# Performance work log

Measured on AMD Instinct MI355X. Metric: run time of the kernel, lower is better.

Reference implementation:

```python
import jax, jax.numpy as jnp
import numpy as np

LN_EPS = 1e-5      # torch.nn.LayerNorm default
NORM_EPS = 1e-12   # torch F.normalize default


def _layernorm(x, gamma, beta):
    mu = jnp.mean(x, axis=-1, keepdims=True)
    var = jnp.mean(jnp.square(x - mu), axis=-1, keepdims=True)
    return (x - mu) * jax.lax.rsqrt(var + LN_EPS) * gamma + beta


def _l2norm(x):
    # normalize over last (embedding) axis, matching F.normalize(dim=1) on [B,E,1,N]
    n = jnp.sqrt(jnp.sum(jnp.square(x), axis=-1, keepdims=True))
    return x / jnp.maximum(n, NORM_EPS)


def setup_inputs() -> dict:
    key = jax.random.key(0)
    ks = jax.random.split(key, 4)
    B, N, C, E = 8, 4096, 768, 768
    x = jax.random.normal(ks[0], (B, N, C), dtype=jnp.float32)
    w_qkv = jax.random.normal(ks[1], (C, 3 * E), dtype=jnp.float32) * (1.0 / np.sqrt(C))
    w_proj = jax.random.normal(ks[2], (E, C), dtype=jnp.float32) * (1.0 / np.sqrt(E))
    ln_in_g = jnp.ones((C,), jnp.float32)
    ln_in_b = jnp.zeros((C,), jnp.float32)
    ln_out_g = jnp.ones((E,), jnp.float32)
    ln_out_b = jnp.zeros((E,), jnp.float32)
    return {"x": x, "w_qkv": w_qkv, "w_proj": w_proj,
            "ln_in_g": ln_in_g, "ln_in_b": ln_in_b,
            "ln_out_g": ln_out_g, "ln_out_b": ln_out_b}


def reference(x, w_qkv, w_proj, ln_in_g, ln_in_b, ln_out_g, ln_out_b):
    # x: [B, N, C]
    h = _layernorm(x, ln_in_g, ln_in_b)
    qkv = h @ w_qkv                                  # [B, N, 3E]
    q, k, v = jnp.split(qkv, 3, axis=-1)             # each [B, N, E]
    phi_q = _l2norm(q)                               # per-token L2 over E
    phi_k = _l2norm(k)
    kv = jnp.sum(phi_k * v, axis=1)                  # [B, E] (sum over tokens N)
    attn = phi_q * kv[:, None, :]                    # [B, N, E]
    out = _layernorm(attn, ln_out_g, ln_out_b) @ w_proj  # [B, N, C]
    return out
```

## Files before the change

### kernel.cpp

```cpp
#include <hip/hip_runtime.h>
#include <hip/hip_bf16.h>
#include <cstdint>

typedef __bf16 bf16;
typedef __bf16 bf16x4 __attribute__((ext_vector_type(4)));
typedef __bf16 bf16x8 __attribute__((ext_vector_type(8)));
typedef float f32x4 __attribute__((ext_vector_type(4)));

#define GK 768
#define LN_EPS 1e-5f
#define NORM_EPS 1e-12f

__device__ __forceinline__ void gl_lds16(const void* g, void* l) {
  __builtin_amdgcn_global_load_lds(
      (__attribute__((address_space(1))) uint32_t*)(uintptr_t)g,
      (__attribute__((address_space(3))) uint32_t*)(uintptr_t)l,
      16, 0, 0);
}

__device__ __forceinline__ void blockReduce2w3(float& s, float& ss, float* sm) {
  #pragma unroll
  for (int o = 32; o > 0; o >>= 1) {
    s  += __shfl_down(s, o, 64);
    ss += __shfl_down(ss, o, 64);
  }
  int wave = threadIdx.x >> 6, lane = threadIdx.x & 63;
  if (lane == 0) { sm[wave] = s; sm[3 + wave] = ss; }
  __syncthreads();
  s  = sm[0] + sm[1] + sm[2];
  ss = sm[3] + sm[4] + sm[5];
  __syncthreads();
}

__global__ __launch_bounds__(256) void transpose_cvt(const float* __restrict__ w,
                                                     bf16* __restrict__ wt,
                                                     int R, int Ncols) {
  __shared__ float tile[32][33];
  int tx = threadIdx.x & 31, ty = threadIdx.x >> 5;
  int c0 = blockIdx.x * 32, r0 = blockIdx.y * 32;
  #pragma unroll
  for (int i = 0; i < 32; i += 8)
    tile[ty + i][tx] = w[(size_t)(r0 + ty + i) * Ncols + (c0 + tx)];
  __syncthreads();
  #pragma unroll
  for (int i = 0; i < 32; i += 8)
    wt[(size_t)(c0 + ty + i) * R + (r0 + tx)] = (bf16)tile[tx][ty + i];
}

__global__ __launch_bounds__(192) void ln_in_kernel(const float* __restrict__ x,
                                                    const float* __restrict__ g,
                                                    const float* __restrict__ b,
                                                    bf16* __restrict__ h) {
  __shared__ float sm[6];
  int row = blockIdx.x, t = threadIdx.x;
  const float* xr = x + (size_t)row * 768;
  float4 v = ((const float4*)xr)[t];
  float s  = v.x + v.y + v.z + v.w;
  float ss = v.x * v.x + v.y * v.y + v.z * v.z + v.w * v.w;
  blockReduce2w3(s, ss, sm);
  float mu  = s * (1.0f / 768.0f);
  float inv = rsqrtf(ss * (1.0f / 768.0f) - mu * mu + LN_EPS);
  float4 gg = ((const float4*)g)[t];
  float4 bb = ((const float4*)b)[t];
  bf16x4 o;
  o[0] = (bf16)((v.x - mu) * inv * gg.x + bb.x);
  o[1] = (bf16)((v.y - mu) * inv * gg.y + bb.y);
  o[2] = (bf16)((v.z - mu) * inv * gg.z + bb.z);
  o[3] = (bf16)((v.w - mu) * inv * gg.w + bb.w);
  ((bf16x4*)(h + (size_t)row * 768))[t] = o;
}


#define SWZ(x) ((x) ^ ((((x) >> 7) & 7) << 4))

#define SB0 __builtin_amdgcn_sched_barrier(0)
#define BARS do { SB0; __builtin_amdgcn_s_barrier(); SB0; } while (0)
#define LGKM(n) do { asm volatile("s_waitcnt lgkmcnt(" #n ")" ::: "memory"); SB0; } while (0)
#define VMC4 do { SB0; asm volatile("s_waitcnt vmcnt(4)" ::: "memory"); } while (0)
#define PRIO1 __builtin_amdgcn_s_setprio(1)
#define PRIO0 __builtin_amdgcn_s_setprio(0)

#define LDA1(base, mh, i, ks) \
  af[i][ks] = *(const bf16x8*)((base) + SWZ((wm * 128 + ((mh) * 4 + (i)) * 16 + llo) * 128 + (ks) * 64 + lhi * 16))

#define LDB1(base, n, ks) \
  bf[n][ks] = *(const bf16x8*)((base) + SWZ(((((n) >> 1) * 128 + wn * 32 + ((n) & 1) * 16 + llo) * 128 + (ks) * 64 + lhi * 16)))

#define MF1(mh, nh, i, jn, ks) \
  acc[(mh) * 4 + (i)][(nh) * 2 + (jn)] = __builtin_amdgcn_mfma_f32_16x16x32_bf16( \
      af[i][ks], bf[(nh) * 2 + (jn)][ks], acc[(mh) * 4 + (i)][(nh) * 2 + (jn)], 0, 0, 0)
#define MF8(mh, nh, ks) do { \
  MF1(mh, nh, 0, 0, ks); MF1(mh, nh, 0, 1, ks); MF1(mh, nh, 1, 0, ks); MF1(mh, nh, 1, 1, ks); \
  MF1(mh, nh, 2, 0, ks); MF1(mh, nh, 2, 1, ks); MF1(mh, nh, 3, 0, ks); MF1(mh, nh, 3, 1, ks); } while (0)

#define STA(b, q, kt) gl_lds16(A + srcA[q] + (kt) * 64, &As_[b][(q) * 4096 + wave * 512])
#define STB(b, q, kt) gl_lds16(Bt + srcB[q] + (kt) * 64, &Bs_[b][(q) * 4096 + wave * 512])

template <bool OUT_BF16>
__global__ __launch_bounds__(512, 2) void gemm8p(const bf16* __restrict__ A,
                                                 const bf16* __restrict__ Bt,
                                                 void* __restrict__ Cv,
                                                 int Nn, int NBN) {
  __shared__ __align__(16) bf16 As_[2][16384];
  __shared__ __align__(16) bf16 Bs_[2][16384];
  const int tid = threadIdx.x;
  const int wave = tid >> 6, lane = tid & 63;
  const int llo = lane & 15, lhi = lane >> 4;
  const int wm = wave >> 2, wn = wave & 3;

  const int nwg = gridDim.x, bid = blockIdx.x;
  const int wg = (bid & 7) * (nwg >> 3) + (bid >> 3);
  const int rb = wg / NBN, cb = wg - rb * NBN;
  const int brow = rb * 256, bcol = cb * 256;

  uint32_t srcA[4], srcB[4];
  #pragma unroll
  for (int q = 0; q < 4; ++q) {
    int d = q * 8192 + tid * 16;
    int a = SWZ(d);
    int r = a >> 7, c = (a & 127) >> 1;
    srcA[q] = (uint32_t)(brow + r) * GK + c;
    int nh = r >> 7, wnn = (r >> 5) & 3, r32 = r & 31;
    srcB[q] = (uint32_t)(bcol + wnn * 64 + nh * 32 + r32) * GK + c;
  }

  f32x4 acc[8][4];
  #pragma unroll
  for (int m = 0; m < 8; ++m)
    #pragma unroll
    for (int n = 0; n < 4; ++n) acc[m][n] = (f32x4){0.f, 0.f, 0.f, 0.f};

  bf16x8 af[4][2], bf[4][2];
  const char* As0 = (const char*)&As_[0][0];
  const char* As1 = (const char*)&As_[1][0];
  const char* Bs0 = (const char*)&Bs_[0][0];
  const char* Bs1 = (const char*)&Bs_[1][0];

  STA(0, 0, 0); STA(0, 1, 0); STA(0, 2, 0); STA(0, 3, 0);
  STB(0, 0, 0); STB(0, 1, 0); STB(0, 2, 0); STB(0, 3, 0);
  STA(1, 0, 1); STA(1, 2, 1); STB(1, 0, 1); STB(1, 1, 1);
  SB0;
  asm volatile("s_waitcnt vmcnt(4)" ::: "memory");
  __builtin_amdgcn_s_barrier();
  SB0;

  for (int j = 0; j < 6; ++j) {
    const int t1 = 2 * j + 1, t2 = 2 * j + 2, t3 = 2 * j + 3;
    LDA1(As0, 0, 0, 0); LDA1(As0, 0, 1, 0); LDA1(As0, 0, 2, 0); LDA1(As0, 0, 3, 0);
    LDB1(Bs0, 0, 0);    LDB1(Bs0, 1, 0);
    SB0;
    LDA1(As0, 0, 0, 1); LDA1(As0, 0, 1, 1); LDA1(As0, 0, 2, 1); LDA1(As0, 0, 3, 1);
    LDB1(Bs0, 0, 1);    LDB1(Bs0, 1, 1);
    SB0;
    LDB1(Bs0, 2, 0); LDB1(Bs0, 3, 0); LDB1(Bs0, 2, 1); LDB1(Bs0, 3, 1);
    STA(1, 1, t1); STA(1, 3, t1);
    BARS;
    LGKM(10); PRIO1; MF8(0, 0, 0);
    LGKM(4);  MF8(0, 0, 1); PRIO0;
    BARS;
    STB(1, 2, t1); STB(1, 3, t1);
    BARS;
    LGKM(0); PRIO1; MF8(0, 1, 0); MF8(0, 1, 1); PRIO0;
    BARS;
    LDA1(As0, 1, 0, 0); LDA1(As0, 1, 1, 0); LDA1(As0, 1, 2, 0); LDA1(As0, 1, 3, 0);
    SB0;
    LDA1(As0, 1, 0, 1); LDA1(As0, 1, 1, 1); LDA1(As0, 1, 2, 1); LDA1(As0, 1, 3, 1);
    STA(0, 0, t2); STA(0, 2, t2);
    BARS;
    LGKM(4); PRIO1; MF8(1, 0, 0);
    LGKM(0); MF8(1, 0, 1); PRIO0;
    BARS;
    STB(0, 0, t2); STB(0, 1, t2);
    BARS;
    PRIO1; MF8(1, 1, 0); MF8(1, 1, 1); PRIO0;
    VMC4;
    BARS;
    LDA1(As1, 0, 0, 0); LDA1(As1, 0, 1, 0); LDA1(As1, 0, 2, 0); LDA1(As1, 0, 3, 0);
    LDB1(Bs1, 0, 0);    LDB1(Bs1, 1, 0);
    SB0;
    LDA1(As1, 0, 0, 1); LDA1(As1, 0, 1, 1); LDA1(As1, 0, 2, 1); LDA1(As1, 0, 3, 1);
    LDB1(Bs1, 0, 1);    LDB1(Bs1, 1, 1);
    SB0;
    LDB1(Bs1, 2, 0); LDB1(Bs1, 3, 0); LDB1(Bs1, 2, 1); LDB1(Bs1, 3, 1);
    STA(0, 1, t2); STA(0, 3, t2);
    BARS;
    LGKM(10); PRIO1; MF8(0, 0, 0);
    LGKM(4);  MF8(0, 0, 1); PRIO0;
    BARS;
    STB(0, 2, t2); STB(0, 3, t2);
    BARS;
    LGKM(0); PRIO1; MF8(0, 1, 0); MF8(0, 1, 1); PRIO0;
    BARS;
    LDA1(As1, 1, 0, 0); LDA1(As1, 1, 1, 0); LDA1(As1, 1, 2, 0); LDA1(As1, 1, 3, 0);
    SB0;
    LDA1(As1, 1, 0, 1); LDA1(As1, 1, 1, 1); LDA1(As1, 1, 2, 1); LDA1(As1, 1, 3, 1);
    STA(1, 0, t3); STA(1, 2, t3);
    BARS;
    LGKM(4); PRIO1; MF8(1, 0, 0);
    LGKM(0); MF8(1, 0, 1); PRIO0;
    BARS;
    STB(1, 0, t3); STB(1, 1, t3);
    BARS;
    PRIO1; MF8(1, 1, 0); MF8(1, 1, 1); PRIO0;
    VMC4;
    BARS;
  }

  #pragma unroll
  for (int m = 0; m < 8; ++m) {
    #pragma unroll
    for (int n = 0; n < 4; ++n) {
      int row = brow + wm * 128 + m * 16 + lhi * 4;
      int col = bcol + wn * 64 + n * 16 + llo;
      #pragma unroll
      for (int r2 = 0; r2 < 4; ++r2) {
        if (OUT_BF16)
          ((bf16*)Cv)[(size_t)(row + r2) * Nn + col] = (bf16)acc[m][n][r2];
        else
          ((float*)Cv)[(size_t)(row + r2) * Nn + col] = acc[m][n][r2];
      }
    }
  }
}

__global__ __launch_bounds__(256) void kv_partial(const bf16* __restrict__ qkv,
                                                  float* __restrict__ kvp) {
  __shared__ float sm[4][768];
  int b = blockIdx.x >> 5, chunk = blockIdx.x & 31;
  int wave = threadIdx.x >> 6, lane = threadIdx.x & 63;
  const bf16* base = qkv + ((size_t)(b * 4096 + chunk * 128 + wave * 32)) * 2304;
  float acc[3][4] = {};
  for (int i = 0; i < 32; ++i) {
    const bf16* kr = base + (size_t)i * 2304 + 768;
    const bf16* vr = kr + 768;
    bf16x4 k4[3], v4[3];
    #pragma unroll
    for (int c = 0; c < 3; ++c) {
      k4[c] = *(const bf16x4*)(kr + c * 256 + lane * 4);
      v4[c] = *(const bf16x4*)(vr + c * 256 + lane * 4);
    }
    float ssk = 0.f;
    #pragma unroll
    for (int c = 0; c < 3; ++c)
      #pragma unroll
      for (int j = 0; j < 4; ++j) { float kf = (float)k4[c][j]; ssk += kf * kf; }
    #pragma unroll
    for (int off = 32; off > 0; off >>= 1) ssk += __shfl_xor(ssk, off, 64);
    float wi = 1.0f / fmaxf(sqrtf(ssk), NORM_EPS);
    #pragma unroll
    for (int c = 0; c < 3; ++c)
      #pragma unroll
      for (int j = 0; j < 4; ++j)
        acc[c][j] += (float)k4[c][j] * (float)v4[c][j] * wi;
  }
  #pragma unroll
  for (int c = 0; c < 3; ++c)
    #pragma unroll
    for (int j = 0; j < 4; ++j)
      sm[wave][c * 256 + lane * 4 + j] = acc[c][j];
  __syncthreads();
  int t = threadIdx.x;
  #pragma unroll
  for (int c = 0; c < 3; ++c) {
    int e = c * 256 + t;
    kvp[(size_t)blockIdx.x * 768 + e] = sm[0][e] + sm[1][e] + sm[2][e] + sm[3][e];
  }
}

__global__ __launch_bounds__(256) void kv_reduce(const float* __restrict__ kvp,
                                                 float* __restrict__ kv) {
  int i = blockIdx.x * 256 + threadIdx.x;
  int b = i / 768, e = i - b * 768;
  float s = 0.f;
  #pragma unroll
  for (int c = 0; c < 32; ++c) s += kvp[(size_t)(b * 32 + c) * 768 + e];
  kv[i] = s;
}

__global__ __launch_bounds__(192) void attn_ln_kernel(const bf16* __restrict__ qkv,
                                                      const float* __restrict__ kv,
                                                      const float* __restrict__ g,
                                                      const float* __restrict__ b,
                                                      bf16* __restrict__ a) {
  __shared__ float sm[6];
  int row = blockIdx.x, t = threadIdx.x;
  int bt = row >> 12;
  const bf16* qr = qkv + (size_t)row * 2304;
  bf16x4 q4 = ((const bf16x4*)qr)[t];
  float q0 = (float)q4[0], q1 = (float)q4[1], q2 = (float)q4[2], q3 = (float)q4[3];
  float sq = q0 * q0 + q1 * q1 + q2 * q2 + q3 * q3, dummy = 0.f;
  blockReduce2w3(sq, dummy, sm);
  float iq = 1.0f / fmaxf(sqrtf(sq), NORM_EPS);
  float4 kv4 = ((const float4*)(kv + bt * 768))[t];
  float4 av;
  av.x = q0 * iq * kv4.x;
  av.y = q1 * iq * kv4.y;
  av.z = q2 * iq * kv4.z;
  av.w = q3 * iq * kv4.w;
  float s  = av.x + av.y + av.z + av.w;
  float ss = av.x * av.x + av.y * av.y + av.z * av.z + av.w * av.w;
  blockReduce2w3(s, ss, sm);
  float mu  = s * (1.0f / 768.0f);
  float inv = rsqrtf(ss * (1.0f / 768.0f) - mu * mu + LN_EPS);
  float4 gg = ((const float4*)g)[t];
  float4 bb = ((const float4*)b)[t];
  bf16x4 o;
  o[0] = (bf16)((av.x - mu) * inv * gg.x + bb.x);
  o[1] = (bf16)((av.y - mu) * inv * gg.y + bb.y);
  o[2] = (bf16)((av.z - mu) * inv * gg.z + bb.z);
  o[3] = (bf16)((av.w - mu) * inv * gg.w + bb.w);
  ((bf16x4*)(a + (size_t)row * 768))[t] = o;
}

extern "C" void kernel_launch(void* const* d_in, const int* in_sizes, int n_in,
                              void* d_out, int out_size, void* d_ws, size_t ws_size,
                              hipStream_t stream) {
  const float* x      = (const float*)d_in[0];
  const float* w_qkv  = (const float*)d_in[1];
  const float* w_proj = (const float*)d_in[2];
  const float* g_in   = (const float*)d_in[3];
  const float* b_in   = (const float*)d_in[4];
  const float* g_out  = (const float*)d_in[5];
  const float* b_out  = (const float*)d_in[6];

  char* ws = (char*)d_ws;
  bf16*  wqkvt  = (bf16*)(ws);
  bf16*  wprojt = (bf16*)(ws + 3538944);
  bf16*  h      = (bf16*)(ws + 4718592);
  bf16*  qkv    = (bf16*)(ws + 55050240);
  float* kvp    = (float*)(ws + 206045184);
  float* kv     = (float*)(ws + 206831616);

  transpose_cvt<<<dim3(2304 / 32, 768 / 32), 256, 0, stream>>>(w_qkv, wqkvt, 768, 2304);
  transpose_cvt<<<dim3(768 / 32, 768 / 32), 256, 0, stream>>>(w_proj, wprojt, 768, 768);
  ln_in_kernel<<<32768, 192, 0, stream>>>(x, g_in, b_in, h);
  gemm8p<true><<<128 * 9, 512, 0, stream>>>(h, wqkvt, (void*)qkv, 2304, 9);
  kv_partial<<<256, 256, 0, stream>>>(qkv, kvp);
  kv_reduce<<<24, 256, 0, stream>>>(kvp, kv);
  attn_ln_kernel<<<32768, 192, 0, stream>>>(qkv, kv, g_out, b_out, h);
  gemm8p<false><<<128 * 3, 512, 0, stream>>>(h, wprojt, d_out, 768, 3);
}
```

Measured before the change: 292.6 us.

## Switch GEMMs to 32x32x16 MFMA and use 128-row tiles for projection

Replaces the 16x16x32 bf16 MFMA tiling in the pipelined GEMM with 32x32x16 MFMAs, changing the LDS fragment loads and the epilogue store mapping to fit. The GEMM is templated on M-tile count, and the output projection now uses 128-row tiles with a simpler double-buffered schedule, doubling its grid to 768 workgroups. The larger MFMA shape is meant to cut LDS fragment traffic per FLOP, and the smaller projection tiles are meant to fill more CUs. The trade-offs are a strided epilogue store pattern and less reuse per tile in the projection GEMM.

```diff
diff --git a/kernel.cpp b/kernel.cpp
--- a/kernel.cpp
+++ b/kernel.cpp
@@ -6,6 +6,7 @@
 typedef __bf16 bf16x4 __attribute__((ext_vector_type(4)));
 typedef __bf16 bf16x8 __attribute__((ext_vector_type(8)));
 typedef float f32x4 __attribute__((ext_vector_type(4)));
+typedef float f32x16 __attribute__((ext_vector_type(16)));
 
 #define GK 768
 #define LN_EPS 1e-5f
@@ -76,148 +77,190 @@
 #define SB0 __builtin_amdgcn_sched_barrier(0)
 #define BARS do { SB0; __builtin_amdgcn_s_barrier(); SB0; } while (0)
 #define LGKM(n) do { asm volatile("s_waitcnt lgkmcnt(" #n ")" ::: "memory"); SB0; } while (0)
-#define VMC4 do { SB0; asm volatile("s_waitcnt vmcnt(4)" ::: "memory"); } while (0)
+#define VMC(n) do { SB0; asm volatile("s_waitcnt vmcnt(" #n ")" ::: "memory"); } while (0)
 #define PRIO1 __builtin_amdgcn_s_setprio(1)
 #define PRIO0 __builtin_amdgcn_s_setprio(0)
 
-#define LDA1(base, mh, i, ks) \
-  af[i][ks] = *(const bf16x8*)((base) + SWZ((wm * 128 + ((mh) * 4 + (i)) * 16 + llo) * 128 + (ks) * 64 + lhi * 16))
-
-#define LDB1(base, n, ks) \
-  bf[n][ks] = *(const bf16x8*)((base) + SWZ(((((n) >> 1) * 128 + wn * 32 + ((n) & 1) * 16 + llo) * 128 + (ks) * 64 + lhi * 16)))
-
-#define MF1(mh, nh, i, jn, ks) \
-  acc[(mh) * 4 + (i)][(nh) * 2 + (jn)] = __builtin_amdgcn_mfma_f32_16x16x32_bf16( \
-      af[i][ks], bf[(nh) * 2 + (jn)][ks], acc[(mh) * 4 + (i)][(nh) * 2 + (jn)], 0, 0, 0)
-#define MF8(mh, nh, ks) do { \
-  MF1(mh, nh, 0, 0, ks); MF1(mh, nh, 0, 1, ks); MF1(mh, nh, 1, 0, ks); MF1(mh, nh, 1, 1, ks); \
-  MF1(mh, nh, 2, 0, ks); MF1(mh, nh, 2, 1, ks); MF1(mh, nh, 3, 0, ks); MF1(mh, nh, 3, 1, ks); } while (0)
+#define LDA32(buf, mh, mi, k) \
+  af[mi][k] = *(const bf16x8*)((buf) + SWZ((wm * (MT * 32) + (mh) * 64 + (mi) * 32 + l31) * 128 + (k) * 32 + g16))
+#define LDB32(buf, nt, k) \
+  bfr[nt][k] = *(const bf16x8*)((buf) + SWZ(((nt) * 128 + wn * 32 + l31) * 128 + (k) * 32 + g16))
+
+#define MFA(mh, mi, nt, k) \
+  acc[(mh) * 2 + (mi)][nt] = __builtin_amdgcn_mfma_f32_32x32x16_bf16( \
+      af[mi][k], bfr[nt][k], acc[(mh) * 2 + (mi)][nt], 0, 0, 0)
+#define MF4(mh, nt, ka, kb) do { \
+  MFA(mh, 0, nt, ka); MFA(mh, 1, nt, ka); MFA(mh, 0, nt, kb); MFA(mh, 1, nt, kb); } while (0)
+
+#define RG_A01(buf, mh) do { LDA32(buf, mh, 0, 0); LDA32(buf, mh, 1, 0); LDA32(buf, mh, 0, 1); LDA32(buf, mh, 1, 1); } while (0)
+#define RG_A23(buf, mh) do { LDA32(buf, mh, 0, 2); LDA32(buf, mh, 1, 2); LDA32(buf, mh, 0, 3); LDA32(buf, mh, 1, 3); } while (0)
+#define RG_B0a(buf) do { LDB32(buf, 0, 0); LDB32(buf, 0, 1); } while (0)
+#define RG_B0b(buf) do { LDB32(buf, 0, 2); LDB32(buf, 0, 3); } while (0)
+#define RG_B1(buf)  do { LDB32(buf, 1, 0); LDB32(buf, 1, 1); LDB32(buf, 1, 2); LDB32(buf, 1, 3); } while (0)
 
 #define STA(b, q, kt) gl_lds16(A + srcA[q] + (kt) * 64, &As_[b][(q) * 4096 + wave * 512])
 #define STB(b, q, kt) gl_lds16(Bt + srcB[q] + (kt) * 64, &Bs_[b][(q) * 4096 + wave * 512])
 
-template <bool OUT_BF16>
+template <int MT, bool OUT_BF16>
 __global__ __launch_bounds__(512, 2) void gemm8p(const bf16* __restrict__ A,
                                                  const bf16* __restrict__ Bt,
                                                  void* __restrict__ Cv,
                                                  int Nn, int NBN) {
-  __shared__ __align__(16) bf16 As_[2][16384];
+  __shared__ __align__(16) bf16 As_[2][MT * 4096];
   __shared__ __align__(16) bf16 Bs_[2][16384];
   const int tid = threadIdx.x;
   const int wave = tid >> 6, lane = tid & 63;
-  const int llo = lane & 15, lhi = lane >> 4;
+  const int l31 = lane & 31, g16 = (lane >> 5) * 16;
   const int wm = wave >> 2, wn = wave & 3;
 
   const int nwg = gridDim.x, bid = blockIdx.x;
   const int wg = (bid & 7) * (nwg >> 3) + (bid >> 3);
   const int rb = wg / NBN, cb = wg - rb * NBN;
-  const int brow = rb * 256, bcol = cb * 256;
-
-  uint32_t srcA[4], srcB[4];
+  const int brow = rb * (MT * 64), bcol = cb * 256;
+
+  uint32_t srcA[MT], srcB[4];
+  #pragma unroll
+  for (int q = 0; q < MT; ++q) {
+    int d = q * 8192 + tid * 16;
+    int a = SWZ(d);
+    int r = a >> 7, c = (a & 127) >> 1;
+    srcA[q] = (uint32_t)(brow + r) * GK + c;
+  }
   #pragma unroll
   for (int q = 0; q < 4; ++q) {
     int d = q * 8192 + tid * 16;
     int a = SWZ(d);
     int r = a >> 7, c = (a & 127) >> 1;
-    srcA[q] = (uint32_t)(brow + r) * GK + c;
     int nh = r >> 7, wnn = (r >> 5) & 3, r32 = r & 31;
     srcB[q] = (uint32_t)(bcol + wnn * 64 + nh * 32 + r32) * GK + c;
   }
 
-  f32x4 acc[8][4];
-  #pragma unroll
-  for (int m = 0; m < 8; ++m)
-    #pragma unroll
-    for (int n = 0; n < 4; ++n) acc[m][n] = (f32x4){0.f, 0.f, 0.f, 0.f};
-
-  bf16x8 af[4][2], bf[4][2];
+  f32x16 acc[MT][2];
+  #pragma unroll
+  for (int m = 0; m < MT; ++m)
+    #pragma unroll
+    for (int n = 0; n < 2; ++n)
+      #pragma unroll
+      for (int r2 = 0; r2 < 16; ++r2) acc[m][n][r2] = 0.f;
+
+  bf16x8 af[2][4], bfr[2][4];
   const char* As0 = (const char*)&As_[0][0];
   const char* As1 = (const char*)&As_[1][0];
   const char* Bs0 = (const char*)&Bs_[0][0];
   const char* Bs1 = (const char*)&Bs_[1][0];
 
-  STA(0, 0, 0); STA(0, 1, 0); STA(0, 2, 0); STA(0, 3, 0);
-  STB(0, 0, 0); STB(0, 1, 0); STB(0, 2, 0); STB(0, 3, 0);
-  STA(1, 0, 1); STA(1, 2, 1); STB(1, 0, 1); STB(1, 1, 1);
-  SB0;
-  asm volatile("s_waitcnt vmcnt(4)" ::: "memory");
-  __builtin_amdgcn_s_barrier();
-  SB0;
-
-  for (int j = 0; j < 6; ++j) {
-    const int t1 = 2 * j + 1, t2 = 2 * j + 2, t3 = 2 * j + 3;
-    LDA1(As0, 0, 0, 0); LDA1(As0, 0, 1, 0); LDA1(As0, 0, 2, 0); LDA1(As0, 0, 3, 0);
-    LDB1(Bs0, 0, 0);    LDB1(Bs0, 1, 0);
+  if constexpr (MT == 4) {
+    STA(0, 0, 0); STA(0, 1, 0); STA(0, 2, 0); STA(0, 3, 0);
+    STB(0, 0, 0); STB(0, 1, 0); STB(0, 2, 0); STB(0, 3, 0);
+    STA(1, 0, 1); STA(1, 2, 1); STB(1, 0, 1); STB(1, 1, 1);
     SB0;
-    LDA1(As0, 0, 0, 1); LDA1(As0, 0, 1, 1); LDA1(As0, 0, 2, 1); LDA1(As0, 0, 3, 1);
-    LDB1(Bs0, 0, 1);    LDB1(Bs0, 1, 1);
+    asm volatile("s_waitcnt vmcnt(4)" ::: "memory");
+    __builtin_amdgcn_s_barrier();
     SB0;
-    LDB1(Bs0, 2, 0); LDB1(Bs0, 3, 0); LDB1(Bs0, 2, 1); LDB1(Bs0, 3, 1);
-    STA(1, 1, t1); STA(1, 3, t1);
-    BARS;
-    LGKM(10); PRIO1; MF8(0, 0, 0);
-    LGKM(4);  MF8(0, 0, 1); PRIO0;
-    BARS;
-    STB(1, 2, t1); STB(1, 3, t1);
-    BARS;
-    LGKM(0); PRIO1; MF8(0, 1, 0); MF8(0, 1, 1); PRIO0;
-    BARS;
-    LDA1(As0, 1, 0, 0); LDA1(As0, 1, 1, 0); LDA1(As0, 1, 2, 0); LDA1(As0, 1, 3, 0);
+
+    for (int j = 0; j < 6; ++j) {
+      const int t1 = 2 * j + 1, t2 = 2 * j + 2, t3 = 2 * j + 3;
+      RG_A01(As0, 0); RG_B0a(Bs0); SB0;
+      RG_A23(As0, 0); RG_B0b(Bs0); SB0;
+      RG_B1(Bs0); SB0;
+      STA(1, 1, t1); STA(1, 3, t1);
+      BARS;
+      LGKM(10); PRIO1; MF4(0, 0, 0, 1);
+      LGKM(4);  MF4(0, 0, 2, 3); PRIO0;
+      BARS;
+      STB(1, 2, t1); STB(1, 3, t1);
+      BARS;
+      LGKM(0); PRIO1; MF4(0, 1, 0, 1); MF4(0, 1, 2, 3); PRIO0;
+      BARS;
+      RG_A01(As0, 1); SB0;
+      RG_A23(As0, 1); SB0;
+      STA(0, 0, t2); STA(0, 2, t2);
+      BARS;
+      LGKM(4); PRIO1; MF4(1, 0, 0, 1);
+      LGKM(0); MF4(1, 0, 2, 3); PRIO0;
+      BARS;
+      STB(0, 0, t2); STB(0, 1, t2);
+      BARS;
+      PRIO1; MF4(1, 1, 0, 1); MF4(1, 1, 2, 3); PRIO0;
+      VMC(4);
+      BARS;
+      RG_A01(As1, 0); RG_B0a(Bs1); SB0;
+      RG_A23(As1, 0); RG_B0b(Bs1); SB0;
+      RG_B1(Bs1); SB0;
+      STA(0, 1, t2); STA(0, 3, t2);
+      BARS;
+      LGKM(10); PRIO1; MF4(0, 0, 0, 1);
+      LGKM(4);  MF4(0, 0, 2, 3); PRIO0;
+      BARS;
+      STB(0, 2, t2); STB(0, 3, t2);
+      BARS;
+      LGKM(0); PRIO1; MF4(0, 1, 0, 1); MF4(0, 1, 2, 3); PRIO0;
+      BARS;
+      RG_A01(As1, 1); SB0;
+      RG_A23(As1, 1); SB0;
+      STA(1, 0, t3); STA(1, 2, t3);
+      BARS;
+      LGKM(4); PRIO1; MF4(1, 0, 0, 1);
+      LGKM(0); MF4(1, 0, 2, 3); PRIO0;
+      BARS;
+      STB(1, 0, t3); STB(1, 1, t3);
+      BARS;
+      PRIO1; MF4(1, 1, 0, 1); MF4(1, 1, 2, 3); PRIO0;
+      VMC(4);
+      BARS;
+    }
+  } else {
+    STA(0, 0, 0); STA(0, 1, 0);
+    STB(0, 0, 0); STB(0, 1, 0); STB(0, 2, 0); STB(0, 3, 0);
     SB0;
-    LDA1(As0, 1, 0, 1); LDA1(As0, 1, 1, 1); LDA1(As0, 1, 2, 1); LDA1(As0, 1, 3, 1);
-    STA(0, 0, t2); STA(0, 2, t2);
-    BARS;
-    LGKM(4); PRIO1; MF8(1, 0, 0);
-    LGKM(0); MF8(1, 0, 1); PRIO0;
-    BARS;
-    STB(0, 0, t2); STB(0, 1, t2);
-    BARS;
-    PRIO1; MF8(1, 1, 0); MF8(1, 1, 1); PRIO0;
-    VMC4;
-    BARS;
-    LDA1(As1, 0, 0, 0); LDA1(As1, 0, 1, 0); LDA1(As1, 0, 2, 0); LDA1(As1, 0, 3, 0);
-    LDB1(Bs1, 0, 0);    LDB1(Bs1, 1, 0);
+    asm volatile("s_waitcnt vmcnt(0)" ::: "memory");
+    __builtin_amdgcn_s_barrier();
     SB0;
-    LDA1(As1, 0, 0, 1); LDA1(As1, 0, 1, 1); LDA1(As1, 0, 2, 1); LDA1(As1, 0, 3, 1);
-    LDB1(Bs1, 0, 1);    LDB1(Bs1, 1, 1);
-    SB0;
-    LDB1(Bs1, 2, 0); LDB1(Bs1, 3, 0); LDB1(Bs1, 2, 1); LDB1(Bs1, 3, 1);
-    STA(0, 1, t2); STA(0, 3, t2);
-    BARS;
-    LGKM(10); PRIO1; MF8(0, 0, 0);
-    LGKM(4);  MF8(0, 0, 1); PRIO0;
-    BARS;
-    STB(0, 2, t2); STB(0, 3, t2);
-    BARS;
-    LGKM(0); PRIO1; MF8(0, 1, 0); MF8(0, 1, 1); PRIO0;
-    BARS;
-    LDA1(As1, 1, 0, 0); LDA1(As1, 1, 1, 0); LDA1(As1, 1, 2, 0); LDA1(As1, 1, 3, 0);
-    SB0;
-    LDA1(As1, 1, 0, 1); LDA1(As1, 1, 1, 1); LDA1(As1, 1, 2, 1); LDA1(As1, 1, 3, 1);
-    STA(1, 0, t3); STA(1, 2, t3);
-    BARS;
-    LGKM(4); PRIO1; MF8(1, 0, 0);
-    LGKM(0); MF8(1, 0, 1); PRIO0;
-    BARS;
-    STB(1, 0, t3); STB(1, 1, t3);
-    BARS;
-    PRIO1; MF8(1, 1, 0); MF8(1, 1, 1); PRIO0;
-    VMC4;
-    BARS;
-  }
-
-  #pragma unroll
-  for (int m = 0; m < 8; ++m) {
-    #pragma unroll
-    for (int n = 0; n < 4; ++n) {
-      int row = brow + wm * 128 + m * 16 + lhi * 4;
-      int col = bcol + wn * 64 + n * 16 + llo;
+
+    for (int j = 0; j < 6; ++j) {
+      const int t1 = 2 * j + 1, t2 = 2 * j + 2;
+      RG_A01(As0, 0); RG_B0a(Bs0); SB0;
+      RG_A23(As0, 0); RG_B0b(Bs0); SB0;
+      RG_B1(Bs0); SB0;
+      STA(1, 0, t1); STA(1, 1, t1);
+      STB(1, 0, t1); STB(1, 1, t1); STB(1, 2, t1); STB(1, 3, t1);
+      BARS;
+      LGKM(10); PRIO1; MF4(0, 0, 0, 1);
+      LGKM(4);  MF4(0, 0, 2, 3); PRIO0;
+      BARS;
+      BARS;
+      LGKM(0); PRIO1; MF4(0, 1, 0, 1); MF4(0, 1, 2, 3); PRIO0;
+      VMC(0);
+      BARS;
+      RG_A01(As1, 0); RG_B0a(Bs1); SB0;
+      RG_A23(As1, 0); RG_B0b(Bs1); SB0;
+      RG_B1(Bs1); SB0;
+      STA(0, 0, t2); STA(0, 1, t2);
+      STB(0, 0, t2); STB(0, 1, t2); STB(0, 2, t2); STB(0, 3, t2);
+      BARS;
+      LGKM(10); PRIO1; MF4(0, 0, 0, 1);
+      LGKM(4);  MF4(0, 0, 2, 3); PRIO0;
+      BARS;
+      BARS;
+      LGKM(0); PRIO1; MF4(0, 1, 0, 1); MF4(0, 1, 2, 3); PRIO0;
+      VMC(0);
+      BARS;
+    }
+  }
+
+  #pragma unroll
+  for (int mt = 0; mt < MT; ++mt) {
+    #pragma unroll
+    for (int nt = 0; nt < 2; ++nt) {
+      int col = bcol + wn * 64 + nt * 32 + l31;
+      int row0 = brow + wm * (MT * 32) + mt * 32 + (g16 >> 2);
       #pragma unroll
-      for (int r2 = 0; r2 < 4; ++r2) {
+      for (int rg = 0; rg < 16; ++rg) {
+        int row = row0 + (rg & 3) + 8 * (rg >> 2);
         if (OUT_BF16)
-          ((bf16*)Cv)[(size_t)(row + r2) * Nn + col] = (bf16)acc[m][n][r2];
+          ((bf16*)Cv)[(size_t)row * Nn + col] = (bf16)acc[mt][nt][rg];
         else
-          ((float*)Cv)[(size_t)(row + r2) * Nn + col] = acc[m][n][r2];
+          ((float*)Cv)[(size_t)row * Nn + col] = acc[mt][nt][rg];
       }
     }
   }
@@ -334,9 +377,9 @@
   transpose_cvt<<<dim3(2304 / 32, 768 / 32), 256, 0, stream>>>(w_qkv, wqkvt, 768, 2304);
   transpose_cvt<<<dim3(768 / 32, 768 / 32), 256, 0, stream>>>(w_proj, wprojt, 768, 768);
   ln_in_kernel<<<32768, 192, 0, stream>>>(x, g_in, b_in, h);
-  gemm8p<true><<<128 * 9, 512, 0, stream>>>(h, wqkvt, (void*)qkv, 2304, 9);
+  gemm8p<4, true><<<128 * 9, 512, 0, stream>>>(h, wqkvt, (void*)qkv, 2304, 9);
   kv_partial<<<256, 256, 0, stream>>>(qkv, kvp);
   kv_reduce<<<24, 256, 0, stream>>>(kvp, kv);
   attn_ln_kernel<<<32768, 192, 0, stream>>>(qkv, kv, g_out, b_out, h);
-  gemm8p<false><<<128 * 3, 512, 0, stream>>>(h, wprojt, d_out, 768, 3);
-}
+  gemm8p<2, false><<<256 * 3, 512, 0, stream>>>(h, wprojt, d_out, 768, 3);
+}
```

Measured after the change: 301.9 us. 3.2% more time.

## Double-buffer GEMM register fragments to overlap LDS reads with MFMA

Applied to the files above, without the earlier changes.

Restructures the 256x256 GEMM main loop so that A and B fragments are kept in two register sets (a0s/a1s, b0s/b1s). The next quadrant's LDS reads and the global-to-LDS prefetches are issued before the current quadrant's 16 MFMAs, so shared-memory read latency is hidden behind matrix math instead of waited on. Barriers drop from four to two per quadrant and the vmcnt waits are retuned. The extra fragment registers raise VGPR pressure under the two-workgroup launch bound, and the reordered wait points must still keep buffer reuse correct.

```diff
diff --git a/kernel.cpp b/kernel.cpp
--- a/kernel.cpp
+++ b/kernel.cpp
@@ -75,23 +75,35 @@
 
 #define SB0 __builtin_amdgcn_sched_barrier(0)
 #define BARS do { SB0; __builtin_amdgcn_s_barrier(); SB0; } while (0)
-#define LGKM(n) do { asm volatile("s_waitcnt lgkmcnt(" #n ")" ::: "memory"); SB0; } while (0)
-#define VMC4 do { SB0; asm volatile("s_waitcnt vmcnt(4)" ::: "memory"); } while (0)
+#define LGKM0 do { asm volatile("s_waitcnt lgkmcnt(0)" ::: "memory"); SB0; } while (0)
+#define VMC(n) do { SB0; asm volatile("s_waitcnt vmcnt(" #n ")" ::: "memory"); } while (0)
 #define PRIO1 __builtin_amdgcn_s_setprio(1)
 #define PRIO0 __builtin_amdgcn_s_setprio(0)
 
-#define LDA1(base, mh, i, ks) \
-  af[i][ks] = *(const bf16x8*)((base) + SWZ((wm * 128 + ((mh) * 4 + (i)) * 16 + llo) * 128 + (ks) * 64 + lhi * 16))
-
-#define LDB1(base, n, ks) \
-  bf[n][ks] = *(const bf16x8*)((base) + SWZ(((((n) >> 1) * 128 + wn * 32 + ((n) & 1) * 16 + llo) * 128 + (ks) * 64 + lhi * 16)))
-
-#define MF1(mh, nh, i, jn, ks) \
+#define LDA_(S, i, ks, base, mh) \
+  S[i][ks] = *(const bf16x8*)((base) + SWZ((wm * 128 + (mh) * 64 + (i) * 16 + llo) * 128 + (ks) * 64 + lhi * 16))
+#define RD_A(S, base, mh) do { \
+  LDA_(S, 0, 0, base, mh); LDA_(S, 1, 0, base, mh); LDA_(S, 2, 0, base, mh); LDA_(S, 3, 0, base, mh); \
+  LDA_(S, 0, 1, base, mh); LDA_(S, 1, 1, base, mh); LDA_(S, 2, 1, base, mh); LDA_(S, 3, 1, base, mh); } while (0)
+
+#define LDB_(S, jn, ks, base, nh) \
+  S[jn][ks] = *(const bf16x8*)((base) + SWZ(((nh) * 128 + wn * 32 + (jn) * 16 + llo) * 128 + (ks) * 64 + lhi * 16))
+#define RD_B(S, base, nh) do { \
+  LDB_(S, 0, 0, base, nh); LDB_(S, 1, 0, base, nh); LDB_(S, 0, 1, base, nh); LDB_(S, 1, 1, base, nh); } while (0)
+
+#define MF1v(AS, BS, mh, nh, i, jn, ks) \
   acc[(mh) * 4 + (i)][(nh) * 2 + (jn)] = __builtin_amdgcn_mfma_f32_16x16x32_bf16( \
-      af[i][ks], bf[(nh) * 2 + (jn)][ks], acc[(mh) * 4 + (i)][(nh) * 2 + (jn)], 0, 0, 0)
-#define MF8(mh, nh, ks) do { \
-  MF1(mh, nh, 0, 0, ks); MF1(mh, nh, 0, 1, ks); MF1(mh, nh, 1, 0, ks); MF1(mh, nh, 1, 1, ks); \
-  MF1(mh, nh, 2, 0, ks); MF1(mh, nh, 2, 1, ks); MF1(mh, nh, 3, 0, ks); MF1(mh, nh, 3, 1, ks); } while (0)
+      AS[i][ks], BS[jn][ks], acc[(mh) * 4 + (i)][(nh) * 2 + (jn)], 0, 0, 0)
+#define MF16(AS, BS, mh, nh) do { PRIO1; \
+  MF1v(AS, BS, mh, nh, 0, 0, 0); MF1v(AS, BS, mh, nh, 0, 1, 0); \
+  MF1v(AS, BS, mh, nh, 1, 0, 0); MF1v(AS, BS, mh, nh, 1, 1, 0); \
+  MF1v(AS, BS, mh, nh, 2, 0, 0); MF1v(AS, BS, mh, nh, 2, 1, 0); \
+  MF1v(AS, BS, mh, nh, 3, 0, 0); MF1v(AS, BS, mh, nh, 3, 1, 0); \
+  MF1v(AS, BS, mh, nh, 0, 0, 1); MF1v(AS, BS, mh, nh, 0, 1, 1); \
+  MF1v(AS, BS, mh, nh, 1, 0, 1); MF1v(AS, BS, mh, nh, 1, 1, 1); \
+  MF1v(AS, BS, mh, nh, 2, 0, 1); MF1v(AS, BS, mh, nh, 2, 1, 1); \
+  MF1v(AS, BS, mh, nh, 3, 0, 1); MF1v(AS, BS, mh, nh, 3, 1, 1); \
+  PRIO0; } while (0)
 
 #define STA(b, q, kt) gl_lds16(A + srcA[q] + (kt) * 64, &As_[b][(q) * 4096 + wave * 512])
 #define STB(b, q, kt) gl_lds16(Bt + srcB[q] + (kt) * 64, &Bs_[b][(q) * 4096 + wave * 512])
@@ -130,7 +142,7 @@
     #pragma unroll
     for (int n = 0; n < 4; ++n) acc[m][n] = (f32x4){0.f, 0.f, 0.f, 0.f};
 
-  bf16x8 af[4][2], bf[4][2];
+  bf16x8 a0s[4][2], a1s[4][2], b0s[2][2], b1s[2][2];
   const char* As0 = (const char*)&As_[0][0];
   const char* As1 = (const char*)&As_[1][0];
   const char* Bs0 = (const char*)&Bs_[0][0];
@@ -143,66 +155,54 @@
   asm volatile("s_waitcnt vmcnt(4)" ::: "memory");
   __builtin_amdgcn_s_barrier();
   SB0;
+  RD_A(a0s, As0, 0); RD_B(b0s, Bs0, 0);
+  SB0;
 
   for (int j = 0; j < 6; ++j) {
     const int t1 = 2 * j + 1, t2 = 2 * j + 2, t3 = 2 * j + 3;
-    LDA1(As0, 0, 0, 0); LDA1(As0, 0, 1, 0); LDA1(As0, 0, 2, 0); LDA1(As0, 0, 3, 0);
-    LDB1(Bs0, 0, 0);    LDB1(Bs0, 1, 0);
-    SB0;
-    LDA1(As0, 0, 0, 1); LDA1(As0, 0, 1, 1); LDA1(As0, 0, 2, 1); LDA1(As0, 0, 3, 1);
-    LDB1(Bs0, 0, 1);    LDB1(Bs0, 1, 1);
-    SB0;
-    LDB1(Bs0, 2, 0); LDB1(Bs0, 3, 0); LDB1(Bs0, 2, 1); LDB1(Bs0, 3, 1);
-    STA(1, 1, t1); STA(1, 3, t1);
-    BARS;
-    LGKM(10); PRIO1; MF8(0, 0, 0);
-    LGKM(4);  MF8(0, 0, 1); PRIO0;
-    BARS;
-    STB(1, 2, t1); STB(1, 3, t1);
-    BARS;
-    LGKM(0); PRIO1; MF8(0, 1, 0); MF8(0, 1, 1); PRIO0;
-    BARS;
-    LDA1(As0, 1, 0, 0); LDA1(As0, 1, 1, 0); LDA1(As0, 1, 2, 0); LDA1(As0, 1, 3, 0);
-    SB0;
-    LDA1(As0, 1, 0, 1); LDA1(As0, 1, 1, 1); LDA1(As0, 1, 2, 1); LDA1(As0, 1, 3, 1);
-    STA(0, 0, t2); STA(0, 2, t2);
-    BARS;
-    LGKM(4); PRIO1; MF8(1, 0, 0);
-    LGKM(0); MF8(1, 0, 1); PRIO0;
-    BARS;
-    STB(0, 0, t2); STB(0, 1, t2);
-    BARS;
-    PRIO1; MF8(1, 1, 0); MF8(1, 1, 1); PRIO0;
-    VMC4;
-    BARS;
-    LDA1(As1, 0, 0, 0); LDA1(As1, 0, 1, 0); LDA1(As1, 0, 2, 0); LDA1(As1, 0, 3, 0);
-    LDB1(Bs1, 0, 0);    LDB1(Bs1, 1, 0);
-    SB0;
-    LDA1(As1, 0, 0, 1); LDA1(As1, 0, 1, 1); LDA1(As1, 0, 2, 1); LDA1(As1, 0, 3, 1);
-    LDB1(Bs1, 0, 1);    LDB1(Bs1, 1, 1);
-    SB0;
-    LDB1(Bs1, 2, 0); LDB1(Bs1, 3, 0); LDB1(Bs1, 2, 1); LDB1(Bs1, 3, 1);
-    STA(0, 1, t2); STA(0, 3, t2);
-    BARS;
-    LGKM(10); PRIO1; MF8(0, 0, 0);
-    LGKM(4);  MF8(0, 0, 1); PRIO0;
-    BARS;
-    STB(0, 2, t2); STB(0, 3, t2);
-    BARS;
-    LGKM(0); PRIO1; MF8(0, 1, 0); MF8(0, 1, 1); PRIO0;
-    BARS;
-    LDA1(As1, 1, 0, 0); LDA1(As1, 1, 1, 0); LDA1(As1, 1, 2, 0); LDA1(As1, 1, 3, 0);
-    SB0;
-    LDA1(As1, 1, 0, 1); LDA1(As1, 1, 1, 1); LDA1(As1, 1, 2, 1); LDA1(As1, 1, 3, 1);
-    STA(1, 0, t3); STA(1, 2, t3);
-    BARS;
-    LGKM(4); PRIO1; MF8(1, 0, 0);
-    LGKM(0); MF8(1, 0, 1); PRIO0;
-    BARS;
-    STB(1, 0, t3); STB(1, 1, t3);
-    BARS;
-    PRIO1; MF8(1, 1, 0); MF8(1, 1, 1); PRIO0;
-    VMC4;
+    LGKM0;
+    RD_B(b1s, Bs0, 1); SB0;
+    STA(1, 1, t1); STA(1, 3, t1); SB0;
+    MF16(a0s, b0s, 0, 0);
+    BARS;
+    LGKM0;
+    RD_A(a1s, As0, 1); SB0;
+    STB(1, 2, t1); STB(1, 3, t1); SB0;
+    MF16(a0s, b1s, 0, 1);
+    VMC(4);
+    BARS;
+    LGKM0;
+    RD_A(a0s, As1, 0); SB0;
+    STA(0, 0, t2); STA(0, 2, t2); SB0;
+    MF16(a1s, b0s, 1, 0);
+    VMC(2);
+    BARS;
+    LGKM0;
+    RD_B(b0s, Bs1, 0); SB0;
+    STB(0, 0, t2); STB(0, 1, t2); SB0;
+    MF16(a1s, b1s, 1, 1);
+    BARS;
+    LGKM0;
+    RD_B(b1s, Bs1, 1); SB0;
+    STA(0, 1, t2); STA(0, 3, t2); SB0;
+    MF16(a0s, b0s, 0, 0);
+    BARS;
+    LGKM0;
+    RD_A(a1s, As1, 1); SB0;
+    STB(0, 2, t2); STB(0, 3, t2); SB0;
+    MF16(a0s, b1s, 0, 1);
+    VMC(4);
+    BARS;
+    LGKM0;
+    RD_A(a0s, As0, 0); SB0;
+    STA(1, 0, t3); STA(1, 2, t3); SB0;
+    MF16(a1s, b0s, 1, 0);
+    VMC(2);
+    BARS;
+    LGKM0;
+    RD_B(b0s, Bs0, 0); SB0;
+    STB(1, 0, t3); STB(1, 1, t3); SB0;
+    MF16(a1s, b1s, 1, 1);
     BARS;
   }
 
```

Result: slower. 613.5 us (+109.6%).
